# Optimization experiments

Hardware: AMD Instinct MI355X
Metric: run time of the kernel (lower is better)

The kernel has to match this reference:

```python
import jax, jax.numpy as jnp
import numpy as np

N, B, HID, NPG, DEG, N_HOPS = 102400, 512, 256, 200, 32, 2
E = N * DEG
LN_EPS = 1e-5


def setup_inputs() -> dict:
    key = jax.random.key(0)
    ks = jax.random.split(key, 8)
    h = jax.random.normal(ks[0], (N, HID), jnp.float32)
    g = jax.random.normal(ks[1], (B, HID), jnp.float32)
    # sorted node->graph assignment, 200 nodes per graph
    batch = jnp.repeat(jnp.arange(B, dtype=jnp.int32), NPG)
    # intra-graph random edges: graph id per edge + local endpoints
    gid = jax.random.randint(ks[2], (E,), 0, B, jnp.int32)
    s_loc = jax.random.randint(ks[3], (E,), 0, NPG, jnp.int32)
    d_loc = jax.random.randint(ks[4], (E,), 0, NPG, jnp.int32)
    edge_index = jnp.stack([gid * NPG + s_loc, gid * NPG + d_loc])  # [2, E]
    # head MLP params: Linear(HID,2HID) -> LayerNorm(2HID) -> ReLU -> Linear(2HID,1)
    W1 = jax.random.normal(ks[5], (HID, 2 * HID), jnp.float32) * (1.0 / np.sqrt(HID))
    b1 = jnp.zeros((2 * HID,), jnp.float32)
    ln_g = jnp.ones((2 * HID,), jnp.float32)
    ln_b = jnp.zeros((2 * HID,), jnp.float32)
    W2 = jax.random.normal(ks[6], (2 * HID, 1), jnp.float32) * (1.0 / np.sqrt(2 * HID))
    b2 = jnp.zeros((1,), jnp.float32)
    return {"h": h, "g": g, "batch": batch, "edge_index": edge_index,
            "W1": W1, "b1": b1, "ln_g": ln_g, "ln_b": ln_b, "W2": W2, "b2": b2}


def reference(h, g, batch, edge_index, W1, b1, ln_g, ln_b, W2, b2):
    n = h.shape[0]
    nb = g.shape[0]
    # repeat_interleave(g, bincount(batch)) == g[batch] for sorted batch
    x = h + g[batch]                                   # [N, HID]
    z = x @ W1 + b1                                    # [N, 2*HID]
    mu = jnp.mean(z, axis=-1, keepdims=True)
    var = jnp.var(z, axis=-1, keepdims=True)           # biased, as torch LayerNorm
    z = (z - mu) * jax.lax.rsqrt(var + LN_EPS) * ln_g + ln_b
    z = jax.nn.relu(z)
    logits = (z @ W2 + b2)[:, 0]                       # [N]
    # segment softmax over each graph
    m = jax.ops.segment_max(logits, batch, num_segments=nb)
    e = jnp.exp(logits - m[batch])
    s = jax.ops.segment_sum(e, batch, num_segments=nb)
    node_prob = e / s[batch]                           # [N]
    pmax = jax.ops.segment_max(node_prob, batch, num_segments=nb)
    cand = jnp.where(node_prob >= pmax[batch], jnp.arange(n, dtype=jnp.int32), n)
    seed = jax.ops.segment_min(cand, batch, num_segments=nb)   # [B] global node ids
    # k_hop_subgraph BFS (PyG flow='source_to_target': expand target -> source)
    src, dst = edge_index[0], edge_index[1]
    nm = jnp.zeros((n,), jnp.int32).at[seed].set(1)
    for _ in range(N_HOPS):
        nm = jnp.maximum(nm, jnp.zeros((n,), jnp.int32).at[src].max(nm[dst]))
    nmb = nm > 0
    edge_mask = nmb[src] & nmb[dst]                    # [E] kept-edge mask
    edge_weight = logits[src] + logits[dst]            # [E]
    em = edge_mask.astype(jnp.int32)
    node_mask = (jnp.zeros((n,), jnp.int32).at[src].max(em).at[dst].max(em)) > 0
    return node_prob, edge_weight, edge_mask, node_mask
```

## Files before the change

### kernel.cpp

```cpp
#include <hip/hip_runtime.h>
#include <hip/hip_bf16.h>

#define HID 256
#define HID2 512
#define NPG 200
#define LN_EPS 1e-5f

typedef float f32x4 __attribute__((ext_vector_type(4)));
typedef short s16x8 __attribute__((ext_vector_type(8)));
typedef unsigned short ushort_t;

__device__ __forceinline__ ushort_t f2bf_rne(float x) {
    union { float f; unsigned int u; } c; c.f = x;
    unsigned int u = c.u;
    return (ushort_t)((u + 0x7fffu + ((u >> 16) & 1u)) >> 16);
}
__device__ __forceinline__ float bf2f(ushort_t h) {
    union { unsigned int u; float f; } c; c.u = ((unsigned int)h) << 16;
    return c.f;
}

__global__ __launch_bounds__(256)
void w1_prep_kernel(const float* __restrict__ W1,
                    ushort_t* __restrict__ w1h, ushort_t* __restrict__ w1l)
{
    const int c = blockIdx.x;
    const int k = threadIdx.x;
    const float v = W1[(size_t)k * HID2 + c];
    const ushort_t hi = f2bf_rne(v);
    const float resid = v - bf2f(hi);
    const ushort_t lo = f2bf_rne(resid);
    w1h[(size_t)c * HID + k] = hi;
    w1l[(size_t)c * HID + k] = lo;
}

__global__ __launch_bounds__(512, 4)
void mlp_logits_mfma(const float* __restrict__ h, const float* __restrict__ g,
                     const int* __restrict__ batch,
                     const ushort_t* __restrict__ w1h, const ushort_t* __restrict__ w1l,
                     const float* __restrict__ b1,
                     const float* __restrict__ lng, const float* __restrict__ lnb,
                     const float* __restrict__ W2, const float* __restrict__ b2,
                     float* __restrict__ logits)
{
    __shared__ ushort_t xsh[64 * 256];
    __shared__ ushort_t xsl[64 * 256];
    __shared__ float prm[4 * 512];
    __shared__ float redS1[8][64];
    __shared__ float redS2[8][64];
    __shared__ float redT[8][64];
    __shared__ float muv[64], rsv[64];

    const int tid  = threadIdx.x;
    const int row0 = blockIdx.x * 64;

    {
        const int c = tid;
        prm[c]        = b1[c];
        prm[512 + c]  = lng[c];
        prm[1024 + c] = lnb[c];
        prm[1536 + c] = W2[c];
    }

    #pragma unroll
    for (int i = 0; i < 4; ++i) {
        const int ci = tid + (i << 9);
        const int r  = ci >> 5;
        const int kc = (ci & 31) << 3;
        const int grow = row0 + r;
        const int gb   = batch[grow];
        const float4* hp = reinterpret_cast<const float4*>(h + (size_t)grow * HID + kc);
        const float4* gp = reinterpret_cast<const float4*>(g + (size_t)gb   * HID + kc);
        const float4 h0 = hp[0], h1 = hp[1];
        const float4 g0 = gp[0], g1 = gp[1];
        float xv[8] = { h0.x + g0.x, h0.y + g0.y, h0.z + g0.z, h0.w + g0.w,
                        h1.x + g1.x, h1.y + g1.y, h1.z + g1.z, h1.w + g1.w };
        ushort_t hh[8], ll[8];
        #pragma unroll
        for (int j = 0; j < 8; ++j) {
            const ushort_t hi = f2bf_rne(xv[j]);
            hh[j] = hi;
            ll[j] = f2bf_rne(xv[j] - bf2f(hi));
        }
        int byte_off = r * 512 + (kc << 1);
        byte_off ^= (r & 7) << 4;
        *reinterpret_cast<s16x8*>(reinterpret_cast<char*>(xsh) + byte_off) =
            *reinterpret_cast<const s16x8*>(hh);
        *reinterpret_cast<s16x8*>(reinterpret_cast<char*>(xsl) + byte_off) =
            *reinterpret_cast<const s16x8*>(ll);
    }
    __syncthreads();

    const int w  = tid >> 6;
    const int l  = tid & 63;
    const int lc = l & 15;
    const int gq = l >> 4;
    const int wcol0 = w << 6;

    f32x4 acc[4][4];
    #pragma unroll
    for (int rt = 0; rt < 4; ++rt)
        #pragma unroll
        for (int ct = 0; ct < 4; ++ct) acc[rt][ct] = (f32x4){0.f, 0.f, 0.f, 0.f};

    const size_t bbase = (size_t)(wcol0 + lc) * HID + (gq << 3);

    for (int k0 = 0; k0 < HID; k0 += 32) {
        s16x8 bh[4], bl[4];
        #pragma unroll
        for (int ct = 0; ct < 4; ++ct) {
            const size_t boff = bbase + (size_t)ct * (16 * HID) + k0;
            bh[ct] = *reinterpret_cast<const s16x8*>(w1h + boff);
            bl[ct] = *reinterpret_cast<const s16x8*>(w1l + boff);
        }
        s16x8 ah[4], al[4];
        #pragma unroll
        for (int rt = 0; rt < 4; ++rt) {
            const int arow = (rt << 4) | lc;
            int abyte = arow * 512 + ((k0 + (gq << 3)) << 1);
            abyte ^= (arow & 7) << 4;
            ah[rt] = *reinterpret_cast<const s16x8*>(
                         reinterpret_cast<const char*>(xsh) + abyte);
            al[rt] = *reinterpret_cast<const s16x8*>(
                         reinterpret_cast<const char*>(xsl) + abyte);
        }
        #pragma unroll
        for (int ct = 0; ct < 4; ++ct) {
            #pragma unroll
            for (int rt = 0; rt < 4; ++rt) {
                acc[rt][ct] = __builtin_amdgcn_mfma_f32_16x16x32_bf16(ah[rt], bh[ct], acc[rt][ct], 0, 0, 0);
                acc[rt][ct] = __builtin_amdgcn_mfma_f32_16x16x32_bf16(al[rt], bh[ct], acc[rt][ct], 0, 0, 0);
                acc[rt][ct] = __builtin_amdgcn_mfma_f32_16x16x32_bf16(ah[rt], bl[ct], acc[rt][ct], 0, 0, 0);
            }
        }
    }

    #pragma unroll
    for (int rt = 0; rt < 4; ++rt) {
        float s1[4] = {0.f, 0.f, 0.f, 0.f};
        float s2[4] = {0.f, 0.f, 0.f, 0.f};
        #pragma unroll
        for (int ct = 0; ct < 4; ++ct) {
            const float bb = prm[wcol0 + (ct << 4) + lc];
            #pragma unroll
            for (int reg = 0; reg < 4; ++reg) {
                const float v = acc[rt][ct][reg] + bb;
                acc[rt][ct][reg] = v;
                s1[reg] += v;
                s2[reg] = fmaf(v, v, s2[reg]);
            }
        }
        #pragma unroll
        for (int reg = 0; reg < 4; ++reg) {
            float a = s1[reg], q = s2[reg];
            a += __shfl_xor(a, 1); q += __shfl_xor(q, 1);
            a += __shfl_xor(a, 2); q += __shfl_xor(q, 2);
            a += __shfl_xor(a, 4); q += __shfl_xor(q, 4);
            a += __shfl_xor(a, 8); q += __shfl_xor(q, 8);
            if (lc == 0) {
                const int row = (rt << 4) + (gq << 2) + reg;
                redS1[w][row] = a;
                redS2[w][row] = q;
            }
        }
    }
    __syncthreads();

    if (tid < 64) {
        float S1 = 0.f, S2 = 0.f;
        #pragma unroll
        for (int i = 0; i < 8; ++i) { S1 += redS1[i][tid]; S2 += redS2[i][tid]; }
        const float mu = S1 * (1.0f / HID2);
        const float var = S2 * (1.0f / HID2) - mu * mu;
        muv[tid] = mu;
        rsv[tid] = rsqrtf(var + LN_EPS);
    }
    __syncthreads();

    #pragma unroll
    for (int rt = 0; rt < 4; ++rt) {
        float tpart[4] = {0.f, 0.f, 0.f, 0.f};
        float mus[4], rss[4];
        #pragma unroll
        for (int reg = 0; reg < 4; ++reg) {
            const int row = (rt << 4) + (gq << 2) + reg;
            mus[reg] = muv[row];
            rss[reg] = rsv[row];
        }
        #pragma unroll
        for (int ct = 0; ct < 4; ++ct) {
            const int c = wcol0 + (ct << 4) + lc;
            const float lg = prm[512 + c], lb = prm[1024 + c], w2 = prm[1536 + c];
            #pragma unroll
            for (int reg = 0; reg < 4; ++reg) {
                float zn = (acc[rt][ct][reg] - mus[reg]) * rss[reg] * lg + lb;
                zn = fmaxf(zn, 0.f);
                tpart[reg] = fmaf(zn, w2, tpart[reg]);
            }
        }
        #pragma unroll
        for (int reg = 0; reg < 4; ++reg) {
            float t = tpart[reg];
            t += __shfl_xor(t, 1); t += __shfl_xor(t, 2);
            t += __shfl_xor(t, 4); t += __shfl_xor(t, 8);
            if (lc == 0) redT[w][(rt << 4) + (gq << 2) + reg] = t;
        }
    }
    __syncthreads();

    if (tid < 64) {
        float t = 0.f;
        #pragma unroll
        for (int i = 0; i < 8; ++i) t += redT[i][tid];
        logits[row0 + tid] = t + b2[0];
    }
}

__global__ __launch_bounds__(256)
void softmax_seed_kernel(const float* __restrict__ logits,
                         float* __restrict__ out_prob,
                         unsigned char* __restrict__ nm)
{
    const int gid  = blockIdx.x;
    const int tid  = threadIdx.x;
    const int node = gid * NPG + tid;
    const bool act = tid < NPG;

    __shared__ float redf[4];
    __shared__ int   redi[4];

    float l = act ? logits[node] : -INFINITY;

    float m = l;
    #pragma unroll
    for (int off = 32; off >= 1; off >>= 1) m = fmaxf(m, __shfl_xor(m, off));
    if ((tid & 63) == 0) redf[tid >> 6] = m;
    __syncthreads();
    const float bm = fmaxf(fmaxf(redf[0], redf[1]), fmaxf(redf[2], redf[3]));
    __syncthreads();

    const float e = act ? expf(l - bm) : 0.0f;
    float s = e;
    #pragma unroll
    for (int off = 32; off >= 1; off >>= 1) s += __shfl_xor(s, off);
    if ((tid & 63) == 0) redf[tid >> 6] = s;
    __syncthreads();
    const float bs = redf[0] + redf[1] + redf[2] + redf[3];
    __syncthreads();

    const float p = act ? e / bs : -1.0f;
    if (act) out_prob[node] = p;

    float pm = p;
    #pragma unroll
    for (int off = 32; off >= 1; off >>= 1) pm = fmaxf(pm, __shfl_xor(pm, off));
    if ((tid & 63) == 0) redf[tid >> 6] = pm;
    __syncthreads();
    const float bpm = fmaxf(fmaxf(redf[0], redf[1]), fmaxf(redf[2], redf[3]));

    int c = (act && p >= bpm) ? node : 0x7FFFFFFF;
    #pragma unroll
    for (int off = 32; off >= 1; off >>= 1) c = min(c, __shfl_xor(c, off));
    if ((tid & 63) == 0) redi[tid >> 6] = c;
    __syncthreads();
    if (tid == 0) {
        const int seed = min(min(redi[0], redi[1]), min(redi[2], redi[3]));
        nm[seed] = 1;
    }
}

__global__ __launch_bounds__(256)
void bfs_pass_kernel(const int* __restrict__ ei, unsigned char* __restrict__ nm,
                     const int E, const int maxlvl, const int newlvl)
{
    const int stride = gridDim.x * blockDim.x;
    for (int e = blockIdx.x * blockDim.x + threadIdx.x; e < E; e += stride) {
        const int d  = ei[E + e];
        const int lv = nm[d];
        if (lv >= 1 && lv <= maxlvl) {
            const int s = ei[e];
            if (nm[s] == 0) nm[s] = (unsigned char)newlvl;
        }
    }
}

__global__ __launch_bounds__(256)
void edge_out_kernel(const int* __restrict__ ei, const float* __restrict__ logits,
                     const unsigned char* __restrict__ nm,
                     float* __restrict__ out_ew,
                     float* __restrict__ out_em,
                     unsigned char* __restrict__ nodemask, const int E)
{
    const int stride = gridDim.x * blockDim.x;
    for (int e = blockIdx.x * blockDim.x + threadIdx.x; e < E; e += stride) {
        const int s = ei[e];
        const int d = ei[E + e];
        const float lw = logits[s] + logits[d];
        const bool em  = (nm[s] != 0) && (nm[d] != 0);
        out_ew[e] = lw;
        out_em[e] = em ? 1.0f : 0.0f;
        if (em) { nodemask[s] = 1; nodemask[d] = 1; }
    }
}

__global__ __launch_bounds__(256)
void node_mask_kernel(const unsigned char* __restrict__ nodemask,
                      float* __restrict__ out_nm, const int N)
{
    const int stride = gridDim.x * blockDim.x;
    for (int i = blockIdx.x * blockDim.x + threadIdx.x; i < N; i += stride)
        out_nm[i] = nodemask[i] ? 1.0f : 0.0f;
}

__global__ __launch_bounds__(256)
void zero_ws_kernel(uint4* __restrict__ p, const int n16)
{
    const int i = blockIdx.x * blockDim.x + threadIdx.x;
    if (i < n16) p[i] = make_uint4(0u, 0u, 0u, 0u);
}

extern "C" void kernel_launch(void* const* d_in, const int* in_sizes, int n_in,
                              void* d_out, int out_size, void* d_ws, size_t ws_size,
                              hipStream_t stream)
{
    const float* h     = (const float*)d_in[0];
    const float* g     = (const float*)d_in[1];
    const int*   batch = (const int*)d_in[2];
    const int*   ei    = (const int*)d_in[3];
    const float* W1    = (const float*)d_in[4];
    const float* b1    = (const float*)d_in[5];
    const float* lng   = (const float*)d_in[6];
    const float* lnb   = (const float*)d_in[7];
    const float* W2    = (const float*)d_in[8];
    const float* b2    = (const float*)d_in[9];

    const int N = in_sizes[2];
    const int E = in_sizes[3] / 2;

    float* out        = (float*)d_out;
    float* out_prob   = out;
    float* out_ew     = out + N;
    float* out_em     = out + (size_t)N + E;
    float* out_nmask  = out + (size_t)N + 2 * (size_t)E;

    char* ws = (char*)d_ws;
    float*         logits   = (float*)ws;
    ushort_t*      w1h      = (ushort_t*)(ws + (size_t)N * 4);
    ushort_t*      w1l      = (ushort_t*)(ws + (size_t)N * 4 + 262144);
    unsigned char* nm       = (unsigned char*)(ws + (size_t)N * 4 + 524288);
    unsigned char* nodemask = nm + N;

    const int n16 = (2 * N) / 16;
    zero_ws_kernel<<<(n16 + 255) / 256, 256, 0, stream>>>((uint4*)nm, n16);

    w1_prep_kernel<<<HID2, HID, 0, stream>>>(W1, w1h, w1l);

    mlp_logits_mfma<<<N / 64, 512, 0, stream>>>(h, g, batch, w1h, w1l,
                                                b1, lng, lnb, W2, b2, logits);
    softmax_seed_kernel<<<N / NPG, 256, 0, stream>>>(logits, out_prob, nm);
    bfs_pass_kernel<<<4096, 256, 0, stream>>>(ei, nm, E, 1, 2);
    bfs_pass_kernel<<<4096, 256, 0, stream>>>(ei, nm, E, 2, 3);
    edge_out_kernel<<<4096, 256, 0, stream>>>(ei, logits, nm, out_ew, out_em,
                                              nodemask, E);
    node_mask_kernel<<<512, 256, 0, stream>>>(nodemask, out_nmask, N);
}
```

Measured before the change: 251.3 us.

## Pre-swizzle W1 bf16 split into MFMA fragment order and reorder MFMA chains

```diff
diff --git a/kernel.cpp b/kernel.cpp
--- a/kernel.cpp
+++ b/kernel.cpp
@@ -24,14 +24,16 @@
 void w1_prep_kernel(const float* __restrict__ W1,
                     ushort_t* __restrict__ w1h, ushort_t* __restrict__ w1l)
 {
-    const int c = blockIdx.x;
-    const int k = threadIdx.x;
-    const float v = W1[(size_t)k * HID2 + c];
+    const int col = blockIdx.x;
+    const int k   = threadIdx.x;
+    const float v = W1[(size_t)k * HID2 + col];
     const ushort_t hi = f2bf_rne(v);
-    const float resid = v - bf2f(hi);
-    const ushort_t lo = f2bf_rne(resid);
-    w1h[(size_t)c * HID + k] = hi;
-    w1l[(size_t)c * HID + k] = lo;
+    const ushort_t lo = f2bf_rne(v - bf2f(hi));
+    const int tile = col >> 4, lc = col & 15;
+    const int kq = k >> 5, gq = (k >> 3) & 3, j = k & 7;
+    const size_t idx = ((((size_t)tile << 3) + kq) * 64 + (gq << 4) + lc) * 8 + j;
+    w1h[idx] = hi;
+    w1l[idx] = lo;
 }
 
 __global__ __launch_bounds__(512, 4)
@@ -103,21 +105,22 @@
         #pragma unroll
         for (int ct = 0; ct < 4; ++ct) acc[rt][ct] = (f32x4){0.f, 0.f, 0.f, 0.f};
 
-    const size_t bbase = (size_t)(wcol0 + lc) * HID + (gq << 3);
-
-    for (int k0 = 0; k0 < HID; k0 += 32) {
+    const ushort_t* bfh = w1h + (((size_t)w << 2) << 3) * 512 + (size_t)l * 8;
+    const ushort_t* bfl = w1l + (((size_t)w << 2) << 3) * 512 + (size_t)l * 8;
+
+    for (int kq = 0; kq < 8; ++kq) {
         s16x8 bh[4], bl[4];
         #pragma unroll
         for (int ct = 0; ct < 4; ++ct) {
-            const size_t boff = bbase + (size_t)ct * (16 * HID) + k0;
-            bh[ct] = *reinterpret_cast<const s16x8*>(w1h + boff);
-            bl[ct] = *reinterpret_cast<const s16x8*>(w1l + boff);
+            const size_t foff = (size_t)((ct << 3) + kq) * 512;
+            bh[ct] = *reinterpret_cast<const s16x8*>(bfh + foff);
+            bl[ct] = *reinterpret_cast<const s16x8*>(bfl + foff);
         }
         s16x8 ah[4], al[4];
         #pragma unroll
         for (int rt = 0; rt < 4; ++rt) {
             const int arow = (rt << 4) | lc;
-            int abyte = arow * 512 + ((k0 + (gq << 3)) << 1);
+            int abyte = arow * 512 + (((kq << 5) + (gq << 3)) << 1);
             abyte ^= (arow & 7) << 4;
             ah[rt] = *reinterpret_cast<const s16x8*>(
                          reinterpret_cast<const char*>(xsh) + abyte);
@@ -125,14 +128,20 @@
                          reinterpret_cast<const char*>(xsl) + abyte);
         }
         #pragma unroll
-        for (int ct = 0; ct < 4; ++ct) {
-            #pragma unroll
-            for (int rt = 0; rt < 4; ++rt) {
+        for (int ct = 0; ct < 4; ++ct)
+            #pragma unroll
+            for (int rt = 0; rt < 4; ++rt)
                 acc[rt][ct] = __builtin_amdgcn_mfma_f32_16x16x32_bf16(ah[rt], bh[ct], acc[rt][ct], 0, 0, 0);
+        #pragma unroll
+        for (int ct = 0; ct < 4; ++ct)
+            #pragma unroll
+            for (int rt = 0; rt < 4; ++rt)
                 acc[rt][ct] = __builtin_amdgcn_mfma_f32_16x16x32_bf16(al[rt], bh[ct], acc[rt][ct], 0, 0, 0);
+        #pragma unroll
+        for (int ct = 0; ct < 4; ++ct)
+            #pragma unroll
+            for (int rt = 0; rt < 4; ++rt)
                 acc[rt][ct] = __builtin_amdgcn_mfma_f32_16x16x32_bf16(ah[rt], bl[ct], acc[rt][ct], 0, 0, 0);
-            }
-        }
     }
 
     #pragma unroll
```

New measurement: 233.1 us. 7.2% less time.
